# Kernel optimization log

Hardware: AMD Instinct MI355X
Metric: run time of the kernel (lower is better)

## Reference

```python
import jax, jax.numpy as jnp
import numpy as np

N_NODES = 100000
N_EDGES = 25000
NNZ = 800000
D_IN = 256
D_OUT = 256


def setup_inputs() -> dict:
    key = jax.random.key(0)
    k1, k2, k3, k4, k5, k6, k7 = jax.random.split(key, 7)
    return {
        "input": jax.random.normal(k1, (N_NODES, D_IN), dtype=jnp.float32),
        "V": jax.random.randint(k2, (NNZ,), 0, N_NODES, dtype=jnp.int32),
        "E": jax.random.randint(k3, (NNZ,), 0, N_EDGES, dtype=jnp.int32),
        "degV": jax.random.uniform(k4, (N_NODES, 1), dtype=jnp.float32),
        "degE": jax.random.uniform(k5, (N_EDGES, 1), dtype=jnp.float32),
        "weight": jax.random.normal(k6, (D_IN, D_OUT), dtype=jnp.float32) / np.sqrt(D_OUT),
        "bias": jax.random.normal(k7, (D_OUT,), dtype=jnp.float32) / np.sqrt(D_OUT),
    }


def reference(input, V, E, degV, degE, weight, bias):
    num_nodes = degV.shape[0]
    num_edges = degE.shape[0]
    # dense projection: [N, D_in] @ [D_in, D_out]
    X = input @ weight
    # vertex -> edge: gather per-incidence node feats, scatter-mean into edges
    Xve = X[V]  # [nnz, D_out]
    esum = jax.ops.segment_sum(Xve, E, num_segments=num_edges)
    ecnt = jax.ops.segment_sum(jnp.ones((E.shape[0], 1), X.dtype), E, num_segments=num_edges)
    Xe = esum / jnp.maximum(ecnt, 1.0)  # scatter mean
    Xe = Xe * degE  # edge degree scaling
    # edge -> vertex: gather edge feats, scatter-sum into nodes
    Xev = Xe[E]  # [nnz, D_out]
    Xv = jax.ops.segment_sum(Xev, V, num_segments=num_nodes)
    return Xv * degV + bias
```

## Files before the change

kernel.cpp:

```cpp
#include <hip/hip_runtime.h>
#include <stdint.h>

#define N_NODES 100000
#define N_EDGES 25000
#define NNZ_    800000
#define D       256
#define NTOT    (N_EDGES + N_NODES)
#define MP      25024

#define SHE   9
#define SHV   11
#define WKE   512
#define WKV   2048
#define NBKE  ((N_EDGES + WKE - 1) / WKE)
#define NBKV  ((N_NODES + WKV - 1) / WKV)
#define NB    (NBKE + NBKV)
#define CAP   24576

#define SC1B ((NNZ_ / 16 + 255) / 256)
#define WB 256
#define CB ((N_NODES * D / 8 + 255) / 256)

typedef short  short8   __attribute__((ext_vector_type(8)));
typedef float  f32x4    __attribute__((ext_vector_type(4)));
typedef ushort ushortx8 __attribute__((ext_vector_type(8)));
typedef ushort ushortx4 __attribute__((ext_vector_type(4)));

__device__ __forceinline__ ushort f2bf(float f) {
    uint32_t u = __float_as_uint(f);
    uint32_t r = u + 0x7fffu + ((u >> 16) & 1u);
    return (ushort)(r >> 16);
}
__device__ __forceinline__ float bf2f(ushort u) {
    return __uint_as_float(((uint32_t)u) << 16);
}


__global__ void zero_gcur(int* __restrict__ gcur) {
    gcur[threadIdx.x] = 0;
}


__global__ void __launch_bounds__(256) front_kernel(const int* __restrict__ V,
                                                    const int* __restrict__ E,
                                                    int* __restrict__ gcur,
                                                    int2* __restrict__ pairs,
                                                    const float* __restrict__ W,
                                                    ushort* __restrict__ WT,
                                                    const float* __restrict__ in,
                                                    ushort* __restrict__ Xbf) {
    __shared__ int cnt[NB], base[NB], lcur[NB];
    int b = blockIdx.x, t = threadIdx.x;
    if (b < SC1B) {
        for (int j = t; j < NB; j += 256) cnt[j] = 0;
        __syncthreads();
        int i0 = (b * 256 + t) * 16;
        bool act = i0 < NNZ_;
        if (act) {
#pragma unroll
            for (int c = 0; c < 16; c += 4) {
                int4 e = *reinterpret_cast<const int4*>(E + i0 + c);
                int4 v = *reinterpret_cast<const int4*>(V + i0 + c);
                atomicAdd(&cnt[e.x >> SHE], 1);
                atomicAdd(&cnt[e.y >> SHE], 1);
                atomicAdd(&cnt[e.z >> SHE], 1);
                atomicAdd(&cnt[e.w >> SHE], 1);
                atomicAdd(&cnt[NBKE + (v.x >> SHV)], 1);
                atomicAdd(&cnt[NBKE + (v.y >> SHV)], 1);
                atomicAdd(&cnt[NBKE + (v.z >> SHV)], 1);
                atomicAdd(&cnt[NBKE + (v.w >> SHV)], 1);
            }
        }
        __syncthreads();
        for (int j = t; j < NB; j += 256) {
            int c = cnt[j];
            base[j] = c ? atomicAdd(&gcur[j], c) : 0;
            lcur[j] = 0;
        }
        __syncthreads();
        if (act) {
#pragma unroll
            for (int c = 0; c < 16; c += 4) {
                int4 e = *reinterpret_cast<const int4*>(E + i0 + c);
                int4 v = *reinterpret_cast<const int4*>(V + i0 + c);
                int ev[4] = {e.x, e.y, e.z, e.w};
                int vv[4] = {v.x, v.y, v.z, v.w};
#pragma unroll
                for (int k = 0; k < 4; ++k) {
                    int b1 = ev[k] >> SHE;
                    int p1 = base[b1] + atomicAdd(&lcur[b1], 1);
                    if (p1 < CAP) pairs[(size_t)b1 * CAP + p1] = make_int2(ev[k], vv[k]);
                    int b2 = NBKE + (vv[k] >> SHV);
                    int p2 = base[b2] + atomicAdd(&lcur[b2], 1);
                    if (p2 < CAP) pairs[(size_t)b2 * CAP + p2] = make_int2(vv[k], ev[k]);
                }
            }
        }
    } else if (b < SC1B + WB) {
        int g = (b - SC1B) * 256 + t;
        int n = g >> 8, k = g & 255;
        WT[(size_t)n * 256 + k] = f2bf(W[(size_t)k * 256 + n]);
    } else {
        int i = (b - SC1B - WB) * 256 + t;
        if (i >= N_NODES * D / 8) return;
        const f32x4* p = reinterpret_cast<const f32x4*>(in) + (size_t)i * 2;
        f32x4 a = __builtin_nontemporal_load(p);
        f32x4 c = __builtin_nontemporal_load(p + 1);
        ushortx8 o;
        o[0] = f2bf(a[0]); o[1] = f2bf(a[1]); o[2] = f2bf(a[2]); o[3] = f2bf(a[3]);
        o[4] = f2bf(c[0]); o[5] = f2bf(c[1]); o[6] = f2bf(c[2]); o[7] = f2bf(c[3]);
        *(reinterpret_cast<ushortx8*>(Xbf) + i) = o;
    }
}


__global__ void __launch_bounds__(256) build_csr(const int2* __restrict__ pairs,
                                                 const int* __restrict__ gcur,
                                                 int* __restrict__ offC,
                                                 int* __restrict__ adjAll) {
    __shared__ int hist[WKV];
    __shared__ int tsum[256];
    __shared__ int bsum_sh[NB];
    __shared__ int bbase_sh;
    int b = blockIdx.x, t = threadIdx.x;
    bool eside = b < NBKE;
    int kb    = eside ? b * WKE : (b - NBKE) * WKV;
    int nk    = eside ? min(WKE, N_EDGES - kb) : min(WKV, N_NODES - kb);
    int obase = eside ? kb : N_EDGES + kb;
    for (int j = t; j < WKV; j += 256) hist[j] = 0;
    if (t < NB) bsum_sh[t] = gcur[t];
    __syncthreads();
    if (t == 0) {
        int s = 0;
        for (int j = 0; j < b; ++j) s += bsum_sh[j];
        bbase_sh = s;
    }
    int n = min(gcur[b], CAP);
    const int2* p = pairs + (size_t)b * CAP;
    for (int i = t; i < n; i += 256) {
        atomicAdd(&hist[p[i].x - kb], 1);
    }
    __syncthreads();
    int bbase = bbase_sh;
    int j0 = t * 8;
    int s = 0;
#pragma unroll
    for (int j = 0; j < 8; ++j) s += hist[j0 + j];
    tsum[t] = s;
    __syncthreads();
    for (int o = 1; o < 256; o <<= 1) {
        int u = (t >= o) ? tsum[t - o] : 0;
        __syncthreads();
        tsum[t] += u;
        __syncthreads();
    }
    int excl = tsum[t] - s;
    int curv[8];
#pragma unroll
    for (int j = 0; j < 8; ++j) {
        int h = hist[j0 + j];
        curv[j] = bbase + excl;
        if (j0 + j < nk) offC[obase + j0 + j] = bbase + excl;
        excl += h;
    }
    __syncthreads();
#pragma unroll
    for (int j = 0; j < 8; ++j) hist[j0 + j] = curv[j];
    if (b == NB - 1 && t == 0) offC[NTOT] = bbase + n;
    __syncthreads();
    for (int i = t; i < n; i += 256) {
        int2 pr = p[i];
        int slot = atomicAdd(&hist[pr.x - kb], 1);
        adjAll[slot] = pr.y;
    }
}


__global__ void edge_agg(const ushort* __restrict__ Xbf, const int* __restrict__ adjAll,
                         const int* __restrict__ offC, const float* __restrict__ degE,
                         ushort* __restrict__ Ye) {
    int gid = blockIdx.x * blockDim.x + threadIdx.x;
    int edge = gid >> 6;
    int lane = gid & 63;
    if (edge >= N_EDGES) return;
    int q  = lane >> 4;
    int c8 = (lane & 15) * 8;
    int b = offC[edge], e = offC[edge + 1];
    int cnt = e - b;
    float s = degE[edge] / (float)(cnt > 1 ? cnt : 1);
#pragma unroll
    for (int panel = 0; panel < 2; ++panel) {
        int pc = panel * 128 + c8;
        float a[8] = {0.f, 0.f, 0.f, 0.f, 0.f, 0.f, 0.f, 0.f};
        for (int c0 = 0; c0 < cnt; c0 += 64) {
            int rem = cnt - c0;
            int li = c0 + min(lane, rem - 1);
            int myidx = adjAll[b + li];
            int lim = min(rem, 64);
            for (int j0 = 0; j0 < lim; j0 += 16) {
                int r0 = __shfl(myidx, j0 + 0  + q, 64);
                int r1 = __shfl(myidx, j0 + 4  + q, 64);
                int r2 = __shfl(myidx, j0 + 8  + q, 64);
                int r3 = __shfl(myidx, j0 + 12 + q, 64);
                ushortx8 x0 = *reinterpret_cast<const ushortx8*>(Xbf + (size_t)r0 * D + pc);
                ushortx8 x1 = *reinterpret_cast<const ushortx8*>(Xbf + (size_t)r1 * D + pc);
                ushortx8 x2 = *reinterpret_cast<const ushortx8*>(Xbf + (size_t)r2 * D + pc);
                ushortx8 x3 = *reinterpret_cast<const ushortx8*>(Xbf + (size_t)r3 * D + pc);
                if (j0 + 0 + q < lim) {
#pragma unroll
                    for (int k = 0; k < 8; ++k) a[k] += bf2f(x0[k]);
                }
                if (j0 + 4 + q < lim) {
#pragma unroll
                    for (int k = 0; k < 8; ++k) a[k] += bf2f(x1[k]);
                }
                if (j0 + 8 + q < lim) {
#pragma unroll
                    for (int k = 0; k < 8; ++k) a[k] += bf2f(x2[k]);
                }
                if (j0 + 12 + q < lim) {
#pragma unroll
                    for (int k = 0; k < 8; ++k) a[k] += bf2f(x3[k]);
                }
            }
        }
#pragma unroll
        for (int k = 0; k < 8; ++k) {
            a[k] += __shfl_xor(a[k], 16, 64);
            a[k] += __shfl_xor(a[k], 32, 64);
        }
        if (q == 0) {
            ushortx8 o;
#pragma unroll
            for (int k = 0; k < 8; ++k) o[k] = f2bf(a[k] * s);
            *reinterpret_cast<ushortx8*>(Ye + (size_t)edge * D + pc) = o;
        }
    }
}


__global__ void __launch_bounds__(256) gemm_mfma(const ushort* __restrict__ A,
                                                 const ushort* __restrict__ WT,
                                                 ushort* __restrict__ C, int M) {
    int wid  = threadIdx.x >> 6;
    int lane = threadIdx.x & 63;
    int row0 = blockIdx.x * 64 + wid * 16;
    int lr  = lane & 15;
    int lk8 = (lane >> 4) * 8;
    f32x4 acc[16];
#pragma unroll
    for (int t = 0; t < 16; ++t) acc[t] = (f32x4){0.f, 0.f, 0.f, 0.f};
    int arow = row0 + lr;
    if (arow >= M) arow = M - 1;
    const ushort* aptr = A + (size_t)arow * D;
#pragma unroll
    for (int k0 = 0; k0 < D; k0 += 32) {
        short8 af = *reinterpret_cast<const short8*>(aptr + k0 + lk8);
#pragma unroll
        for (int t = 0; t < 16; ++t) {
            short8 bf = *reinterpret_cast<const short8*>(
                WT + (size_t)(t * 16 + lr) * D + k0 + lk8);
            acc[t] = __builtin_amdgcn_mfma_f32_16x16x32_bf16(af, bf, acc[t], 0, 0, 0);
        }
    }
    int crow = row0 + (lane >> 4) * 4;
#pragma unroll
    for (int t = 0; t < 16; ++t) {
        int ccol = t * 16 + lr;
#pragma unroll
        for (int r = 0; r < 4; ++r) {
            int rr = crow + r;
            if (rr < M) C[(size_t)rr * D + ccol] = f2bf(acc[t][r]);
        }
    }
}


__device__ __forceinline__ void gather_rows(const ushort* __restrict__ src,
                                            const int* __restrict__ adjAll,
                                            int b, int cnt, int half, int col8,
                                            float a[8], int lane) {
    for (int c0 = 0; c0 < cnt; c0 += 64) {
        int rem = cnt - c0;
        int li = c0 + min(lane, rem - 1);
        int myidx = adjAll[b + li];
        int lim = min(rem, 64);
        for (int j0 = 0; j0 < lim; j0 += 8) {
            int r0 = __shfl(myidx, j0 + 0 + half, 64);
            int r1 = __shfl(myidx, j0 + 2 + half, 64);
            int r2 = __shfl(myidx, j0 + 4 + half, 64);
            int r3 = __shfl(myidx, j0 + 6 + half, 64);
            ushortx8 x0 = *reinterpret_cast<const ushortx8*>(src + (size_t)r0 * D + col8);
            ushortx8 x1 = *reinterpret_cast<const ushortx8*>(src + (size_t)r1 * D + col8);
            ushortx8 x2 = *reinterpret_cast<const ushortx8*>(src + (size_t)r2 * D + col8);
            ushortx8 x3 = *reinterpret_cast<const ushortx8*>(src + (size_t)r3 * D + col8);
            if (j0 + 0 + half < lim) {
#pragma unroll
                for (int k = 0; k < 8; ++k) a[k] += bf2f(x0[k]);
            }
            if (j0 + 2 + half < lim) {
#pragma unroll
                for (int k = 0; k < 8; ++k) a[k] += bf2f(x1[k]);
            }
            if (j0 + 4 + half < lim) {
#pragma unroll
                for (int k = 0; k < 8; ++k) a[k] += bf2f(x2[k]);
            }
            if (j0 + 6 + half < lim) {
#pragma unroll
                for (int k = 0; k < 8; ++k) a[k] += bf2f(x3[k]);
            }
        }
    }
}


__global__ void node_agg(const ushort* __restrict__ Ze, const int* __restrict__ adjAll,
                         const int* __restrict__ offC, const float* __restrict__ degV,
                         const float* __restrict__ bias, float* __restrict__ out) {
    int gid = blockIdx.x * blockDim.x + threadIdx.x;
    int node = gid >> 6;
    int lane = gid & 63;
    if (node >= N_NODES) return;
    int half = lane >> 5;
    int col8 = (lane & 31) * 8;
    int b = offC[N_EDGES + node], e = offC[N_EDGES + node + 1];
    int cnt = e - b;
    float a[8] = {0.f, 0.f, 0.f, 0.f, 0.f, 0.f, 0.f, 0.f};
    gather_rows(Ze, adjAll, b, cnt, half, col8, a, lane);
#pragma unroll
    for (int k = 0; k < 8; ++k) a[k] += __shfl_xor(a[k], 32, 64);
    float dv = degV[node];
    int k0 = half * 4;
    int c = col8 + k0;
    f32x4 b4 = *reinterpret_cast<const f32x4*>(bias + c);
    f32x4 o;
    o[0] = a[k0 + 0] * dv + b4[0];
    o[1] = a[k0 + 1] * dv + b4[1];
    o[2] = a[k0 + 2] * dv + b4[2];
    o[3] = a[k0 + 3] * dv + b4[3];
    __builtin_nontemporal_store(o, reinterpret_cast<f32x4*>(out + (size_t)node * D + c));
}


extern "C" void kernel_launch(void* const* d_in, const int* in_sizes, int n_in,
                              void* d_out, int out_size, void* d_ws, size_t ws_size,
                              hipStream_t stream) {
    const float* input  = (const float*)d_in[0];
    const int*   V      = (const int*)d_in[1];
    const int*   E      = (const int*)d_in[2];
    const float* degV   = (const float*)d_in[3];
    const float* degE   = (const float*)d_in[4];
    const float* weight = (const float*)d_in[5];
    const float* bias   = (const float*)d_in[6];
    float* out = (float*)d_out;

    int* gcur   = (int*)d_ws;
    int* offC   = gcur + 128;
    int* adjAll = offC + (NTOT + 1);
    uintptr_t p = (uintptr_t)(adjAll + 2 * NNZ_);
    p = (p + 255) & ~(uintptr_t)255;
    ushort* Xbf = (ushort*)p;
    ushort* Ye  = Xbf + (size_t)N_NODES * D;
    ushort* Ze  = Ye + (size_t)MP * D;
    ushort* WT  = Ze + (size_t)MP * D;
    int2* pairs = (int2*)Ye;

    zero_gcur<<<1, 128, 0, stream>>>(gcur);

    front_kernel<<<SC1B + WB + CB, 256, 0, stream>>>(V, E, gcur, pairs,
                                                     weight, WT, input, Xbf);

    build_csr<<<NB, 256, 0, stream>>>(pairs, gcur, offC, adjAll);

    edge_agg<<<(N_EDGES * 64 + 255) / 256, 256, 0, stream>>>(Xbf, adjAll, offC, degE, Ye);

    gemm_mfma<<<MP / 64, 256, 0, stream>>>(Ye, WT, Ze, N_EDGES);

    node_agg<<<(N_NODES * 64 + 255) / 256, 256, 0, stream>>>(Ze, adjAll, offC, degV, bias, out);
}
```

Measured before the change: 241.1 us.

## Fuse edge aggregation with the bf16 MFMA projection through shared memory

Merges the edge gather-mean kernel and the MFMA GEMM into one kernel. Each block aggregates 64 edges into a padded LDS tile, then multiplies that tile by W^T and writes Ze directly, so the Ye intermediate no longer round-trips through global memory and one launch is dropped. The cost is parallelism: the aggregation now runs as 391 blocks of 4 waves, each wave handling 16 edges one after another, instead of one wave per edge across ~6250 blocks. That reduces the latency hiding available for the irregular gathers.

```diff
diff --git a/kernel.cpp b/kernel.cpp
--- a/kernel.cpp
+++ b/kernel.cpp
@@ -20,6 +20,8 @@
 #define SC1B ((NNZ_ / 16 + 255) / 256)
 #define WB 256
 #define CB ((N_NODES * D / 8 + 255) / 256)
+
+#define YLD 264
 
 typedef short  short8   __attribute__((ext_vector_type(8)));
 typedef float  f32x4    __attribute__((ext_vector_type(4)));
@@ -176,86 +178,92 @@
 }
 
 
-__global__ void edge_agg(const ushort* __restrict__ Xbf, const int* __restrict__ adjAll,
-                         const int* __restrict__ offC, const float* __restrict__ degE,
-                         ushort* __restrict__ Ye) {
-    int gid = blockIdx.x * blockDim.x + threadIdx.x;
-    int edge = gid >> 6;
-    int lane = gid & 63;
-    if (edge >= N_EDGES) return;
+__global__ void __launch_bounds__(256) edge_gemm(const ushort* __restrict__ Xbf,
+                                                 const int* __restrict__ adjAll,
+                                                 const int* __restrict__ offC,
+                                                 const float* __restrict__ degE,
+                                                 const ushort* __restrict__ WT,
+                                                 ushort* __restrict__ Ze) {
+    __shared__ ushort yt[64][YLD];
+    int wid  = threadIdx.x >> 6;
+    int lane = threadIdx.x & 63;
     int q  = lane >> 4;
     int c8 = (lane & 15) * 8;
-    int b = offC[edge], e = offC[edge + 1];
-    int cnt = e - b;
-    float s = degE[edge] / (float)(cnt > 1 ? cnt : 1);
-#pragma unroll
-    for (int panel = 0; panel < 2; ++panel) {
-        int pc = panel * 128 + c8;
-        float a[8] = {0.f, 0.f, 0.f, 0.f, 0.f, 0.f, 0.f, 0.f};
-        for (int c0 = 0; c0 < cnt; c0 += 64) {
-            int rem = cnt - c0;
-            int li = c0 + min(lane, rem - 1);
-            int myidx = adjAll[b + li];
-            int lim = min(rem, 64);
-            for (int j0 = 0; j0 < lim; j0 += 16) {
-                int r0 = __shfl(myidx, j0 + 0  + q, 64);
-                int r1 = __shfl(myidx, j0 + 4  + q, 64);
-                int r2 = __shfl(myidx, j0 + 8  + q, 64);
-                int r3 = __shfl(myidx, j0 + 12 + q, 64);
-                ushortx8 x0 = *reinterpret_cast<const ushortx8*>(Xbf + (size_t)r0 * D + pc);
-                ushortx8 x1 = *reinterpret_cast<const ushortx8*>(Xbf + (size_t)r1 * D + pc);
-                ushortx8 x2 = *reinterpret_cast<const ushortx8*>(Xbf + (size_t)r2 * D + pc);
-                ushortx8 x3 = *reinterpret_cast<const ushortx8*>(Xbf + (size_t)r3 * D + pc);
-                if (j0 + 0 + q < lim) {
-#pragma unroll
-                    for (int k = 0; k < 8; ++k) a[k] += bf2f(x0[k]);
+    int ebase = blockIdx.x * 64;
+
+    for (int ei = 0; ei < 16; ++ei) {
+        int row  = wid * 16 + ei;
+        int edge = ebase + row;
+        if (edge < N_EDGES) {
+            int b = offC[edge], e = offC[edge + 1];
+            int cnt = e - b;
+            float s = degE[edge] / (float)(cnt > 1 ? cnt : 1);
+#pragma unroll
+            for (int panel = 0; panel < 2; ++panel) {
+                int pc = panel * 128 + c8;
+                float a[8] = {0.f, 0.f, 0.f, 0.f, 0.f, 0.f, 0.f, 0.f};
+                for (int c0 = 0; c0 < cnt; c0 += 64) {
+                    int rem = cnt - c0;
+                    int li = c0 + min(lane, rem - 1);
+                    int myidx = adjAll[b + li];
+                    int lim = min(rem, 64);
+                    for (int j0 = 0; j0 < lim; j0 += 16) {
+                        int r0 = __shfl(myidx, j0 + 0  + q, 64);
+                        int r1 = __shfl(myidx, j0 + 4  + q, 64);
+                        int r2 = __shfl(myidx, j0 + 8  + q, 64);
+                        int r3 = __shfl(myidx, j0 + 12 + q, 64);
+                        ushortx8 x0 = *reinterpret_cast<const ushortx8*>(Xbf + (size_t)r0 * D + pc);
+                        ushortx8 x1 = *reinterpret_cast<const ushortx8*>(Xbf + (size_t)r1 * D + pc);
+                        ushortx8 x2 = *reinterpret_cast<const ushortx8*>(Xbf + (size_t)r2 * D + pc);
+                        ushortx8 x3 = *reinterpret_cast<const ushortx8*>(Xbf + (size_t)r3 * D + pc);
+                        if (j0 + 0 + q < lim) {
+#pragma unroll
+                            for (int k = 0; k < 8; ++k) a[k] += bf2f(x0[k]);
+                        }
+                        if (j0 + 4 + q < lim) {
+#pragma unroll
+                            for (int k = 0; k < 8; ++k) a[k] += bf2f(x1[k]);
+                        }
+                        if (j0 + 8 + q < lim) {
+#pragma unroll
+                            for (int k = 0; k < 8; ++k) a[k] += bf2f(x2[k]);
+                        }
+                        if (j0 + 12 + q < lim) {
+#pragma unroll
+                            for (int k = 0; k < 8; ++k) a[k] += bf2f(x3[k]);
+                        }
+                    }
                 }
-                if (j0 + 4 + q < lim) {
-#pragma unroll
-                    for (int k = 0; k < 8; ++k) a[k] += bf2f(x1[k]);
+#pragma unroll
+                for (int k = 0; k < 8; ++k) {
+                    a[k] += __shfl_xor(a[k], 16, 64);
+                    a[k] += __shfl_xor(a[k], 32, 64);
                 }
-                if (j0 + 8 + q < lim) {
-#pragma unroll
-                    for (int k = 0; k < 8; ++k) a[k] += bf2f(x2[k]);
+                if (q == 0) {
+                    ushortx8 o;
+#pragma unroll
+                    for (int k = 0; k < 8; ++k) o[k] = f2bf(a[k] * s);
+                    *reinterpret_cast<ushortx8*>(&yt[row][pc]) = o;
                 }
-                if (j0 + 12 + q < lim) {
-#pragma unroll
-                    for (int k = 0; k < 8; ++k) a[k] += bf2f(x3[k]);
-                }
-            }
-        }
-#pragma unroll
-        for (int k = 0; k < 8; ++k) {
-            a[k] += __shfl_xor(a[k], 16, 64);
-            a[k] += __shfl_xor(a[k], 32, 64);
-        }
-        if (q == 0) {
-            ushortx8 o;
-#pragma unroll
-            for (int k = 0; k < 8; ++k) o[k] = f2bf(a[k] * s);
-            *reinterpret_cast<ushortx8*>(Ye + (size_t)edge * D + pc) = o;
-        }
-    }
-}
-
-
-__global__ void __launch_bounds__(256) gemm_mfma(const ushort* __restrict__ A,
-                                                 const ushort* __restrict__ WT,
-                                                 ushort* __restrict__ C, int M) {
-    int wid  = threadIdx.x >> 6;
-    int lane = threadIdx.x & 63;
-    int row0 = blockIdx.x * 64 + wid * 16;
+            }
+        } else if (q == 0) {
+#pragma unroll
+            for (int panel = 0; panel < 2; ++panel) {
+                ushortx8 z = {0, 0, 0, 0, 0, 0, 0, 0};
+                *reinterpret_cast<ushortx8*>(&yt[row][panel * 128 + c8]) = z;
+            }
+        }
+    }
+    __syncthreads();
+
     int lr  = lane & 15;
     int lk8 = (lane >> 4) * 8;
     f32x4 acc[16];
 #pragma unroll
     for (int t = 0; t < 16; ++t) acc[t] = (f32x4){0.f, 0.f, 0.f, 0.f};
-    int arow = row0 + lr;
-    if (arow >= M) arow = M - 1;
-    const ushort* aptr = A + (size_t)arow * D;
 #pragma unroll
     for (int k0 = 0; k0 < D; k0 += 32) {
-        short8 af = *reinterpret_cast<const short8*>(aptr + k0 + lk8);
+        short8 af = *reinterpret_cast<const short8*>(&yt[wid * 16 + lr][k0 + lk8]);
 #pragma unroll
         for (int t = 0; t < 16; ++t) {
             short8 bf = *reinterpret_cast<const short8*>(
@@ -263,14 +271,14 @@
             acc[t] = __builtin_amdgcn_mfma_f32_16x16x32_bf16(af, bf, acc[t], 0, 0, 0);
         }
     }
-    int crow = row0 + (lane >> 4) * 4;
+    int crow = ebase + wid * 16 + (lane >> 4) * 4;
 #pragma unroll
     for (int t = 0; t < 16; ++t) {
         int ccol = t * 16 + lr;
 #pragma unroll
         for (int r = 0; r < 4; ++r) {
             int rr = crow + r;
-            if (rr < M) C[(size_t)rr * D + ccol] = f2bf(acc[t][r]);
+            if (rr < N_EDGES) Ze[(size_t)rr * D + ccol] = f2bf(acc[t][r]);
         }
     }
 }
@@ -361,10 +369,10 @@
     uintptr_t p = (uintptr_t)(adjAll + 2 * NNZ_);
     p = (p + 255) & ~(uintptr_t)255;
     ushort* Xbf = (ushort*)p;
-    ushort* Ye  = Xbf + (size_t)N_NODES * D;
-    ushort* Ze  = Ye + (size_t)MP * D;
+    ushort* scr = Xbf + (size_t)N_NODES * D;
+    ushort* Ze  = scr + (size_t)MP * D;
     ushort* WT  = Ze + (size_t)MP * D;
-    int2* pairs = (int2*)Ye;
+    int2* pairs = (int2*)scr;
 
     zero_gcur<<<1, 128, 0, stream>>>(gcur);
 
@@ -373,9 +381,7 @@
 
     build_csr<<<NB, 256, 0, stream>>>(pairs, gcur, offC, adjAll);
 
-    edge_agg<<<(N_EDGES * 64 + 255) / 256, 256, 0, stream>>>(Xbf, adjAll, offC, degE, Ye);
-
-    gemm_mfma<<<MP / 64, 256, 0, stream>>>(Ye, WT, Ze, N_EDGES);
+    edge_gemm<<<MP / 64, 256, 0, stream>>>(Xbf, adjAll, offC, degE, WT, Ze);
 
     node_agg<<<(N_NODES * 64 + 255) / 256, 256, 0, stream>>>(Ze, adjAll, offC, degV, bias, out);
 }
```

Result: slower. 259.2 us (+7.5%).

## Overlap node-side CSR construction with edge aggregation in one launch

Applied to the files above, without the earlier changes.

Splits the CSR build so only edge-side buckets are built before edge aggregation. The node-side buckets are built by extra leading blocks of the edge_agg kernel, so that work runs alongside the edge gather. Buffers are rearranged so the pairs staging area lives in Ze instead of Ye, which avoids a conflict with the Ye writes now running at the same time. The cost is higher shared memory per block for the edge_agg blocks, and the node offsets are written while edge blocks read offC.

```diff
diff --git a/kernel.cpp b/kernel.cpp
--- a/kernel.cpp
+++ b/kernel.cpp
@@ -20,6 +20,7 @@
 #define SC1B ((NNZ_ / 16 + 255) / 256)
 #define WB 256
 #define CB ((N_NODES * D / 8 + 255) / 256)
+#define EBLK ((N_EDGES * 64 + 255) / 256)
 
 typedef short  short8   __attribute__((ext_vector_type(8)));
 typedef float  f32x4    __attribute__((ext_vector_type(4)));
@@ -114,15 +115,13 @@
 }
 
 
-__global__ void __launch_bounds__(256) build_csr(const int2* __restrict__ pairs,
-                                                 const int* __restrict__ gcur,
-                                                 int* __restrict__ offC,
-                                                 int* __restrict__ adjAll) {
-    __shared__ int hist[WKV];
-    __shared__ int tsum[256];
-    __shared__ int bsum_sh[NB];
-    __shared__ int bbase_sh;
-    int b = blockIdx.x, t = threadIdx.x;
+__device__ __forceinline__ void build_bucket(int b, const int2* __restrict__ pairs,
+                                             const int* __restrict__ gcur,
+                                             int* __restrict__ offC,
+                                             int* __restrict__ adjAll,
+                                             int* hist, int* tsum, int* bsum_sh,
+                                             int* bbase_sh) {
+    int t = threadIdx.x;
     bool eside = b < NBKE;
     int kb    = eside ? b * WKE : (b - NBKE) * WKV;
     int nk    = eside ? min(WKE, N_EDGES - kb) : min(WKV, N_NODES - kb);
@@ -133,7 +132,7 @@
     if (t == 0) {
         int s = 0;
         for (int j = 0; j < b; ++j) s += bsum_sh[j];
-        bbase_sh = s;
+        *bbase_sh = s;
     }
     int n = min(gcur[b], CAP);
     const int2* p = pairs + (size_t)b * CAP;
@@ -141,7 +140,7 @@
         atomicAdd(&hist[p[i].x - kb], 1);
     }
     __syncthreads();
-    int bbase = bbase_sh;
+    int bbase = *bbase_sh;
     int j0 = t * 8;
     int s = 0;
 #pragma unroll
@@ -166,7 +165,10 @@
     __syncthreads();
 #pragma unroll
     for (int j = 0; j < 8; ++j) hist[j0 + j] = curv[j];
-    if (b == NB - 1 && t == 0) offC[NTOT] = bbase + n;
+    if (t == 0) {
+        if (b == NBKE - 1) offC[N_EDGES] = bbase + n;
+        if (b == NB - 1)   offC[NTOT]    = bbase + n;
+    }
     __syncthreads();
     for (int i = t; i < n; i += 256) {
         int2 pr = p[i];
@@ -176,10 +178,31 @@
 }
 
 
-__global__ void edge_agg(const ushort* __restrict__ Xbf, const int* __restrict__ adjAll,
-                         const int* __restrict__ offC, const float* __restrict__ degE,
-                         ushort* __restrict__ Ye) {
-    int gid = blockIdx.x * blockDim.x + threadIdx.x;
+__global__ void __launch_bounds__(256) build_edge(const int2* __restrict__ pairs,
+                                                  const int* __restrict__ gcur,
+                                                  int* __restrict__ offC,
+                                                  int* __restrict__ adjAll) {
+    __shared__ int hist[WKV], tsum[256], bsum_sh[NB], bbase_sh;
+    build_bucket(blockIdx.x, pairs, gcur, offC, adjAll, hist, tsum, bsum_sh, &bbase_sh);
+}
+
+
+__global__ void __launch_bounds__(256) edge_agg(const ushort* __restrict__ Xbf,
+                                                const int* __restrict__ adjAll,
+                                                const int* __restrict__ offC,
+                                                const float* __restrict__ degE,
+                                                ushort* __restrict__ Ye,
+                                                const int2* __restrict__ pairs,
+                                                const int* __restrict__ gcur,
+                                                int* __restrict__ offC_w,
+                                                int* __restrict__ adjAll_w) {
+    __shared__ int hist[WKV], tsum[256], bsum_sh[NB], bbase_sh;
+    if (blockIdx.x < NBKV) {
+        build_bucket(NBKE + blockIdx.x, pairs, gcur, offC_w, adjAll_w,
+                     hist, tsum, bsum_sh, &bbase_sh);
+        return;
+    }
+    int gid = (blockIdx.x - NBKV) * 256 + threadIdx.x;
     int edge = gid >> 6;
     int lane = gid & 63;
     if (edge >= N_EDGES) return;
@@ -361,19 +384,20 @@
     uintptr_t p = (uintptr_t)(adjAll + 2 * NNZ_);
     p = (p + 255) & ~(uintptr_t)255;
     ushort* Xbf = (ushort*)p;
-    ushort* Ye  = Xbf + (size_t)N_NODES * D;
+    ushort* WT  = Xbf + (size_t)N_NODES * D;
+    ushort* Ye  = WT + 256 * 256;
     ushort* Ze  = Ye + (size_t)MP * D;
-    ushort* WT  = Ze + (size_t)MP * D;
-    int2* pairs = (int2*)Ye;
+    int2* pairs = (int2*)Ze;
 
     zero_gcur<<<1, 128, 0, stream>>>(gcur);
 
     front_kernel<<<SC1B + WB + CB, 256, 0, stream>>>(V, E, gcur, pairs,
                                                      weight, WT, input, Xbf);
 
-    build_csr<<<NB, 256, 0, stream>>>(pairs, gcur, offC, adjAll);
-
-    edge_agg<<<(N_EDGES * 64 + 255) / 256, 256, 0, stream>>>(Xbf, adjAll, offC, degE, Ye);
+    build_edge<<<NBKE, 256, 0, stream>>>(pairs, gcur, offC, adjAll);
+
+    edge_agg<<<NBKV + EBLK, 256, 0, stream>>>(Xbf, adjAll, offC, degE, Ye,
+                                              pairs, gcur, offC, adjAll);
 
     gemm_mfma<<<MP / 64, 256, 0, stream>>>(Ye, WT, Ze, N_EDGES);
 
```

Measured after the change: 255.1 us. +5.8%, slower.
